# Kernel tuning notes

Measured on AMD Instinct MI355X. Metric: run time of the kernel, lower is better.

The kernel has to match this reference:

```python
import jax, jax.numpy as jnp
import numpy as np

POOL = (4000, 4000, 4000)
N_GO = 12000
N_GENES = 20000
IN_F = 8
F = 64
B = 8
D_ATT = 5
L_DIM = 16
N_LAST = 4000
EPS = 1e-5


def _seg(v, ids, n):
    # v: [B, E, ...] -> segment-sum over axis 1
    return jax.vmap(lambda a: jax.ops.segment_sum(a, ids, num_segments=n))(v)


def _ln_nodes(x, g, b):
    # torch does LayerNorm(N) on x.permute(0,2,1): normalize over the NODE axis
    mu = x.mean(axis=1, keepdims=True)
    var = x.var(axis=1, keepdims=True)
    return (x - mu) * jax.lax.rsqrt(var + EPS) * g[None, :, None] + b[None, :, None]


def _bn(x, g, b):
    # BatchNorm1d, training-mode statistics (biased var); channel axis = 1
    if x.ndim == 2:
        mu = x.mean(axis=0)
        var = x.var(axis=0)
        return (x - mu) * jax.lax.rsqrt(var + EPS) * g + b
    mu = x.mean(axis=(0, 2), keepdims=True)
    var = x.var(axis=(0, 2), keepdims=True)
    return (x - mu) * jax.lax.rsqrt(var + EPS) * g[None, :, None] + b[None, :, None]


def _enc(x, src, dst, n, w_inc, w_s, w_att_in, w_att_s, g, b):
    x_in = x @ w_inc.T                 # [B,n,F]
    x_s = x @ w_s.T
    f1 = w_inc.shape[0]
    # W_att_in([x_src; x_dst]) == x_src @ W[:, :f1].T + x_dst @ W[:, f1:].T (GAT trick)
    a_src = x_in @ w_att_in[0, :f1]    # [B,n]
    a_dst = x_in @ w_att_in[0, f1:]
    v = jnp.exp(jnp.tanh(a_src[:, src] + a_dst[:, dst]))   # [B,E]
    vn = v / _seg(v, src, n)[:, src]                        # row-normalized attention
    x_incoming = _seg(vn[:, :, None] * x_in[:, dst, :], src, n)
    v_s = jax.nn.sigmoid(x_s @ w_att_s[0])                  # [B,n]
    out = x_incoming + x_s * v_s[:, :, None]
    return jax.nn.relu(_ln_nodes(out, g, b))


def _dec(x, src, dst, n_rows, offset, w_out, w_sout, g, b):
    x_out = x @ w_out.T
    x_s = x @ w_sout.T
    deg = jax.ops.segment_sum(jnp.ones(src.shape, x.dtype), src, num_segments=n_rows)
    v = 1.0 / deg[src]                                      # [E]
    x_outgoing = _seg(v[None, :, None] * x_out[:, dst, :], src, n_rows)
    out = x_outgoing.at[:, offset:, :].add(x_s)
    return jax.nn.relu(_ln_nodes(out, g, b))


def _forward(data, t, t_D,
             w_inc0, w_inc1, w_s0, w_s1, w_att_in0, w_att_in1, w_att_s0, w_att_s1,
             gb_g0, gb_b0, gb_g1, gb_b1,
             w_out0, w_out1, w_sout0, w_sout1,
             gbd_g0, gbd_b0, gbd_g1, gbd_b1,
             catt_w, catt_bn_g, catt_bn_b,
             conc_w, b_bn_g, b_bn_b,
             concd_w, bd_bn_g, bd_bn_b,
             lat_w1, lat_bn1_g, lat_bn1_b, lat_w2, lat_bn2_g, lat_bn2_b,
             Ag_row, Ag_col,
             enc_src0, enc_dst0, enc_src1, enc_dst1,
             dec_src0, dec_dst0, dec_src1, dec_dst1):
    # initial SNP->GO sparse embedding, one sparse matrix per input channel
    gathered = data[:, Ag_col]                         # [B,nnz]
    msg0 = gathered[:, :, None] * t.T[None, :, :]      # [B,nnz,IN_F]
    x = _seg(msg0, Ag_row, N_GO)                       # [B,N_GO,IN_F]

    # encoder (attention GCN + pooling)
    x = _enc(x, enc_src0, enc_dst0, N_GO, w_inc0, w_s0, w_att_in0, w_att_s0, gb_g0, gb_b0)
    x = x[:, POOL[0]:, :]
    x = _enc(x, enc_src1, enc_dst1, N_GO - POOL[0], w_inc1, w_s1, w_att_in1, w_att_s1, gb_g1, gb_b1)
    x = x[:, POOL[1]:, :]                              # [B,N_LAST,F]

    atten_out = jax.nn.relu(_bn(x @ catt_w.T, catt_bn_g, catt_bn_b))   # [B,N_LAST,D_ATT]
    inp_out = jax.nn.relu(_bn((x @ conc_w.T)[..., 0], b_bn_g, b_bn_b)) # [B,N_LAST]

    # decoder (degree-normalized unpooling)
    x = _dec(x, dec_src0, dec_dst0, POOL[1] + POOL[2], POOL[1], w_out0, w_sout0, gbd_g0, gbd_b0)
    x = _dec(x, dec_src1, dec_dst1, N_GO, POOL[0], w_out1, w_sout1, gbd_g1, gbd_b1)

    out_D = jax.nn.relu(_bn((x @ concd_w.T)[..., 0], bd_bn_g, bd_bn_b))  # [B,N_GO]
    x_D = _seg(out_D[:, Ag_row] * t_D[None, :], Ag_col, N_GENES)          # [B,N_GENES]

    h = jax.nn.relu(_bn(inp_out @ lat_w1.T, lat_bn1_g, lat_bn1_b))
    latent = jax.nn.relu(_bn(h @ lat_w2.T, lat_bn2_g, lat_bn2_b))         # [B,L_DIM]
    return latent, x_D, atten_out


def setup_inputs():
    rng = np.random.default_rng(0)
    # GO-GO adjacency edges (row-major unique, like coalesce)
    e = np.unique(rng.integers(0, N_GO, 144000).astype(np.int64) * N_GO
                  + rng.integers(0, N_GO, 144000))
    r = (e // N_GO).astype(np.int32)
    c = (e % N_GO).astype(np.int32)
    p0, p1 = POOL[0], POOL[0] + POOL[1]
    m = (r >= p0) & (c >= p0)
    enc_src1, enc_dst1 = r[m] - p0, c[m] - p0
    ti, tj = c, r                                  # edges of A.T
    m0 = (ti >= p0) & (tj >= p1)
    dec_src0, dec_dst0 = ti[m0] - p0, tj[m0] - p1
    m1 = tj >= p0
    dec_src1, dec_dst1 = ti[m1], tj[m1] - p0
    # gene <-> GO incidence
    eg = np.unique(rng.integers(0, N_GO, 240000).astype(np.int64) * N_GENES
                   + rng.integers(0, N_GENES, 240000))
    Ag_row = (eg // N_GENES).astype(np.int32)
    Ag_col = (eg % N_GENES).astype(np.int32)
    nnz = Ag_row.shape[0]

    ks = iter(jax.random.split(jax.random.key(0), 40))

    def nrm(shape, s=0.05):
        return jax.random.normal(next(ks), shape, jnp.float32) * s

    return {
        'data': nrm((B, N_GENES), 1.0),
        't': 1.0 + nrm((IN_F, nnz), 0.1),
        't_D': 1.0 + nrm((nnz,), 0.1),
        'w_inc0': nrm((F, IN_F)), 'w_inc1': nrm((F, F)),
        'w_s0': nrm((F, IN_F)), 'w_s1': nrm((F, F)),
        'w_att_in0': nrm((1, 2 * F)), 'w_att_in1': nrm((1, 2 * F)),
        'w_att_s0': nrm((1, F)), 'w_att_s1': nrm((1, F)),
        'gb_g0': jnp.ones(N_GO), 'gb_b0': jnp.zeros(N_GO),
        'gb_g1': jnp.ones(N_GO - p0), 'gb_b1': jnp.zeros(N_GO - p0),
        'w_out0': nrm((F, F)), 'w_out1': nrm((IN_F, F)),
        'w_sout0': nrm((F, F)), 'w_sout1': nrm((IN_F, F)),
        'gbd_g0': jnp.ones(POOL[1] + POOL[2]), 'gbd_b0': jnp.zeros(POOL[1] + POOL[2]),
        'gbd_g1': jnp.ones(N_GO), 'gbd_b1': jnp.zeros(N_GO),
        'catt_w': nrm((D_ATT, F)), 'catt_bn_g': jnp.ones(N_LAST), 'catt_bn_b': jnp.zeros(N_LAST),
        'conc_w': nrm((1, F)), 'b_bn_g': jnp.ones(N_LAST), 'b_bn_b': jnp.zeros(N_LAST),
        'concd_w': nrm((1, IN_F)), 'bd_bn_g': jnp.ones(N_GO), 'bd_bn_b': jnp.zeros(N_GO),
        'lat_w1': nrm((32, N_LAST)), 'lat_bn1_g': jnp.ones(32), 'lat_bn1_b': jnp.zeros(32),
        'lat_w2': nrm((L_DIM, 32)), 'lat_bn2_g': jnp.ones(L_DIM), 'lat_bn2_b': jnp.zeros(L_DIM),
        'Ag_row': jnp.asarray(Ag_row), 'Ag_col': jnp.asarray(Ag_col),
        'enc_src0': jnp.asarray(r), 'enc_dst0': jnp.asarray(c),
        'enc_src1': jnp.asarray(enc_src1), 'enc_dst1': jnp.asarray(enc_dst1),
        'dec_src0': jnp.asarray(dec_src0), 'dec_dst0': jnp.asarray(dec_dst0),
        'dec_src1': jnp.asarray(dec_src1), 'dec_dst1': jnp.asarray(dec_dst1),
    }


def reference(data, t, t_D,
              w_inc0, w_inc1, w_s0, w_s1, w_att_in0, w_att_in1, w_att_s0, w_att_s1,
              gb_g0, gb_b0, gb_g1, gb_b1,
              w_out0, w_out1, w_sout0, w_sout1,
              gbd_g0, gbd_b0, gbd_g1, gbd_b1,
              catt_w, catt_bn_g, catt_bn_b,
              conc_w, b_bn_g, b_bn_b,
              concd_w, bd_bn_g, bd_bn_b,
              lat_w1, lat_bn1_g, lat_bn1_b, lat_w2, lat_bn2_g, lat_bn2_b,
              Ag_row, Ag_col,
              enc_src0, enc_dst0, enc_src1, enc_dst1,
              dec_src0, dec_dst0, dec_src1, dec_dst1):
    return _forward(data, t, t_D,
                    w_inc0, w_inc1, w_s0, w_s1, w_att_in0, w_att_in1, w_att_s0, w_att_s1,
                    gb_g0, gb_b0, gb_g1, gb_b1,
                    w_out0, w_out1, w_sout0, w_sout1,
                    gbd_g0, gbd_b0, gbd_g1, gbd_b1,
                    catt_w, catt_bn_g, catt_bn_b,
                    conc_w, b_bn_g, b_bn_b,
                    concd_w, bd_bn_g, bd_bn_b,
                    lat_w1, lat_bn1_g, lat_bn1_b, lat_w2, lat_bn2_g, lat_bn2_b,
                    Ag_row, Ag_col,
                    enc_src0, enc_dst0, enc_src1, enc_dst1,
                    dec_src0, dec_dst0, dec_src1, dec_dst1)
```

## Files before the change

kernel.cpp:

```cpp
#include <hip/hip_runtime.h>
#include <math.h>

#define BB 8
#define N_GO 12000
#define N_GENES 20000
#define IN_F 8
#define FF 64
#define D_ATT 5
#define L_DIM 16
#define N_LAST 4000
#define P0_ 4000
#define EPSF 1e-5f

__global__ void k_row_bounds(const int* __restrict__ src, int* __restrict__ rs,
                             int* __restrict__ re, int E) {
    int e = blockIdx.x * 256 + threadIdx.x;
    if (e >= E) return;
    int r = src[e];
    if (e == 0 || src[e - 1] != r) rs[r] = e;
    if (e == E - 1 || src[e + 1] != r) re[r] = e + 1;
}

__global__ void k_gene2go_w(const float* __restrict__ data, const float* __restrict__ t,
                            const int* __restrict__ col, const int* __restrict__ rs,
                            const int* __restrict__ re, float* __restrict__ x0, int nnz) {
    int wid = blockIdx.x * 4 + (threadIdx.x >> 6);
    if (wid >= N_GO) return;
    int lane = threadIdx.x & 63;
    int f = lane & 7, eo = lane >> 3;
    int e0 = rs[wid], e1 = re[wid];
    float acc[BB];
#pragma unroll
    for (int b = 0; b < BB; b++) acc[b] = 0.f;
    for (int e = e0; e < e1; e += 8) {
        int ee = e + eo;
        bool ok = ee < e1;
        int ec = ok ? ee : (e1 - 1);
        int c = col[ec];
        float tv = ok ? t[(size_t)f * nnz + ee] : 0.f;
#pragma unroll
        for (int b = 0; b < BB; b++)
            acc[b] += tv * data[b * N_GENES + c];
    }
#pragma unroll
    for (int b = 0; b < BB; b++) {
        acc[b] += __shfl_xor(acc[b], 8);
        acc[b] += __shfl_xor(acc[b], 16);
        acc[b] += __shfl_xor(acc[b], 32);
    }
    if (lane < IN_F) {
#pragma unroll
        for (int b = 0; b < BB; b++)
            x0[((size_t)b * N_GO + wid) * IN_F + lane] = acc[b];
    }
}

template<int FIN, bool SCAL>
__global__ __launch_bounds__(256, 2)
void k_linear2_att(const float* __restrict__ X, const float* __restrict__ W1,
                   const float* __restrict__ W2, const float* __restrict__ watt,
                   const float* __restrict__ ws, float* __restrict__ Y1,
                   float* __restrict__ Y2, float* __restrict__ ASRC,
                   float* __restrict__ ADST, float* __restrict__ VS,
                   int n_nodes, long xbs, int xoff, int total_waves) {
    __shared__ float w1s[FIN * FF];
    __shared__ float w2s[FIN * FF];
    int lane = threadIdx.x & 63;
    for (int i = threadIdx.x; i < FIN * FF; i += 256) {
        int fo = i / FIN, k = i % FIN;
        w1s[k * FF + fo] = W1[i];
        w2s[k * FF + fo] = W2[i];
    }
    __syncthreads();
    float w1r[FIN], w2r[FIN];
#pragma unroll
    for (int k = 0; k < FIN; k++) {
        w1r[k] = w1s[k * FF + lane];
        w2r[k] = w2s[k * FF + lane];
    }
    float wa = 0.f, wb = 0.f, wc = 0.f;
    if (SCAL) { wa = watt[lane]; wb = watt[FF + lane]; wc = ws[lane]; }
    int wid = blockIdx.x * 4 + (threadIdx.x >> 6);
    for (int n = wid; n < n_nodes; n += total_waves) {
        for (int b = 0; b < BB; b++) {
            const float* xr = X + (size_t)b * xbs + (size_t)(n + xoff) * FIN;
            float a1 = 0.f, a2 = 0.f;
#pragma unroll
            for (int k = 0; k < FIN; k += 4) {
                float4 x = *(const float4*)(xr + k);
                a1 += x.x * w1r[k] + x.y * w1r[k + 1] + x.z * w1r[k + 2] + x.w * w1r[k + 3];
                a2 += x.x * w2r[k] + x.y * w2r[k + 1] + x.z * w2r[k + 2] + x.w * w2r[k + 3];
            }
            Y1[((size_t)b * n_nodes + n) * FF + lane] = a1;
            Y2[((size_t)b * n_nodes + n) * FF + lane] = a2;
            if (SCAL) {
                float s0 = a1 * wa, s1 = a1 * wb, s2 = a2 * wc;
                for (int m = 1; m < 64; m <<= 1) {
                    s0 += __shfl_xor(s0, m);
                    s1 += __shfl_xor(s1, m);
                    s2 += __shfl_xor(s2, m);
                }
                if (lane == 0) {
                    ASRC[b * n_nodes + n] = s0;
                    ADST[b * n_nodes + n] = s1;
                    VS[b * n_nodes + n] = 1.f / (1.f + expf(-s2));
                }
            }
        }
    }
}

__global__ __launch_bounds__(256, 2)
void k_linear2_reg8(const float* __restrict__ X, const float* __restrict__ W1,
                    const float* __restrict__ W2, float* __restrict__ Y1,
                    float* __restrict__ Y2, int n_nodes, long xbs, int xoff,
                    int total_waves) {
    __shared__ float w1s[FF * IN_F];
    __shared__ float w2s[FF * IN_F];
    int lane = threadIdx.x & 63;
    for (int i = threadIdx.x; i < FF * IN_F; i += 256) {
        int fo = i / FF, k = i % FF;
        w1s[k * IN_F + fo] = W1[i];
        w2s[k * IN_F + fo] = W2[i];
    }
    __syncthreads();
    int of = lane & 7;
    int slot = lane >> 3;
    float w1r[FF], w2r[FF];
#pragma unroll
    for (int k = 0; k < FF; k++) {
        w1r[k] = w1s[k * IN_F + of];
        w2r[k] = w2s[k * IN_F + of];
    }
    int wid = blockIdx.x * 4 + (threadIdx.x >> 6);
    for (long n0 = (long)wid * 8; n0 < n_nodes; n0 += (long)total_waves * 8) {
        int n = (int)n0 + slot;
        bool ok = (n < n_nodes);
        int nn = ok ? n : (n_nodes - 1);
        for (int b = 0; b < BB; b++) {
            const float* xr = X + (size_t)b * xbs + (size_t)(nn + xoff) * FF;
            float a1 = 0.f, a2 = 0.f;
#pragma unroll
            for (int k = 0; k < FF; k += 4) {
                float4 x = *(const float4*)(xr + k);
                a1 += x.x * w1r[k] + x.y * w1r[k + 1] + x.z * w1r[k + 2] + x.w * w1r[k + 3];
                a2 += x.x * w2r[k] + x.y * w2r[k + 1] + x.z * w2r[k + 2] + x.w * w2r[k + 3];
            }
            if (ok) {
                Y1[((size_t)b * n_nodes + n) * IN_F + of] = a1;
                Y2[((size_t)b * n_nodes + n) * IN_F + of] = a2;
            }
        }
    }
}

__global__ void k_edge_v(const float* __restrict__ a_src, const float* __restrict__ a_dst,
                         const int* __restrict__ src, const int* __restrict__ dst,
                         float* __restrict__ v, int E, int n_nodes) {
    int e = blockIdx.x * 256 + threadIdx.x;
    if (e >= E) return;
    int b = blockIdx.y;
    v[(size_t)b * E + e] = expf(tanhf(a_src[b * n_nodes + src[e]] + a_dst[b * n_nodes + dst[e]]));
}

__global__ void k_agg_enc_f(const float* __restrict__ Xin, const float* __restrict__ Xs,
                            const float* __restrict__ EDGEV, const float* __restrict__ VS,
                            const int* __restrict__ dst, const int* __restrict__ rs,
                            const int* __restrict__ re, float* __restrict__ Out,
                            float* __restrict__ sums, int n_nodes, int E, int nblk) {
    int b = blockIdx.x & 7;
    int wid = threadIdx.x >> 6;
    int lane = threadIdx.x & 63;
    const float* Xb  = Xin + (size_t)b * n_nodes * FF;
    const float* Xsb = Xs  + (size_t)b * n_nodes * FF;
    const float* vv  = EDGEV + (size_t)b * E;
    float s1 = 0.f, s2 = 0.f;
    for (int r = (blockIdx.x >> 3) * 4 + wid; r < n_nodes; r += nblk * 4) {
        int e0 = rs[r], e1 = re[r];
        float sv0 = 0.f, sv1 = 0.f, acc0 = 0.f, acc1 = 0.f;
        int e = e0;
        for (; e + 1 < e1; e += 2) {
            int d0 = dst[e], d1 = dst[e + 1];
            float v0 = vv[e], v1 = vv[e + 1];
            sv0 += v0; sv1 += v1;
            acc0 += v0 * Xb[(size_t)d0 * FF + lane];
            acc1 += v1 * Xb[(size_t)d1 * FF + lane];
        }
        if (e < e1) {
            int d0 = dst[e];
            float v0 = vv[e];
            sv0 += v0;
            acc0 += v0 * Xb[(size_t)d0 * FF + lane];
        }
        float sv = sv0 + sv1, acc = acc0 + acc1;
        float o = (e1 > e0) ? acc / sv : 0.f;
        o += Xsb[(size_t)r * FF + lane] * VS[b * n_nodes + r];
        Out[((size_t)b * n_nodes + r) * FF + lane] = o;
        s1 += o; s2 += o * o;
    }
    __shared__ float sh1[4][64], sh2[4][64];
    sh1[wid][lane] = s1; sh2[wid][lane] = s2;
    __syncthreads();
    if (wid == 0) {
        float a = sh1[0][lane] + sh1[1][lane] + sh1[2][lane] + sh1[3][lane];
        float c = sh2[0][lane] + sh2[1][lane] + sh2[2][lane] + sh2[3][lane];
        atomicAdd(&sums[(b * FF + lane) * 2],     a);
        atomicAdd(&sums[(b * FF + lane) * 2 + 1], c);
    }
}

__global__ void k_ln_stats(const float* __restrict__ X, float* __restrict__ sums,
                           int n_nodes, int Fdim, int npb) {
    int b = blockIdx.y;
    int f = threadIdx.x & (Fdim - 1);
    int nl = threadIdx.x / Fdim;
    int stride = 256 / Fdim;
    int n0 = blockIdx.x * npb;
    int n1 = n0 + npb; if (n1 > n_nodes) n1 = n_nodes;
    const float* xb = X + (size_t)b * n_nodes * Fdim;
    float s1 = 0.f, s2 = 0.f;
    for (int n = n0 + nl; n < n1; n += stride) {
        float x = xb[(size_t)n * Fdim + f];
        s1 += x; s2 += x * x;
    }
    __shared__ float sh1[256], sh2[256];
    sh1[threadIdx.x] = s1; sh2[threadIdx.x] = s2;
    __syncthreads();
    for (int o = 128; o >= Fdim; o >>= 1) {
        if (threadIdx.x < o) { sh1[threadIdx.x] += sh1[threadIdx.x + o]; sh2[threadIdx.x] += sh2[threadIdx.x + o]; }
        __syncthreads();
    }
    if (threadIdx.x < Fdim) {
        atomicAdd(&sums[(b * Fdim + threadIdx.x) * 2],     sh1[threadIdx.x]);
        atomicAdd(&sums[(b * Fdim + threadIdx.x) * 2 + 1], sh2[threadIdx.x]);
    }
}

__global__ void k_ln_apply_relu(const float* __restrict__ X, const float* __restrict__ sums,
                                const float* __restrict__ g, const float* __restrict__ bb,
                                float* __restrict__ Y, int n_nodes, int Fdim) {
    long idx = (long)blockIdx.x * 256 + threadIdx.x;
    if (idx >= (long)n_nodes * Fdim) return;
    int b = blockIdx.y;
    int n = (int)(idx / Fdim);
    int f = (int)(idx % Fdim);
    float s1 = sums[(b * Fdim + f) * 2], s2 = sums[(b * Fdim + f) * 2 + 1];
    float mu = s1 / n_nodes;
    float var = s2 / n_nodes - mu * mu;
    float rs = rsqrtf(var + EPSF);
    size_t o = (size_t)b * n_nodes * Fdim + idx;
    float y = (X[o] - mu) * rs * g[n] + bb[n];
    Y[o] = fmaxf(y, 0.f);
}

__global__ void k_deg_i(const int* __restrict__ src, int* __restrict__ deg, int E) {
    int e = blockIdx.x * 256 + threadIdx.x;
    if (e < E) atomicAdd(&deg[src[e]], 1);
}

__global__ void k_scan(const int* __restrict__ deg, int* __restrict__ rsd,
                       int* __restrict__ cursor, int n) {
    __shared__ int part[1024];
    int t = threadIdx.x;
    int chunk = (n + 1023) >> 10;
    int s0 = t * chunk, s1 = s0 + chunk; if (s1 > n) s1 = n;
    int s = 0;
    for (int i = s0; i < s1 && i < n; i++) s += deg[i];
    part[t] = s;
    __syncthreads();
    for (int o = 1; o < 1024; o <<= 1) {
        int v = (t >= o) ? part[t - o] : 0;
        __syncthreads();
        part[t] += v;
        __syncthreads();
    }
    int base = (t == 0) ? 0 : part[t - 1];
    for (int i = s0; i < s1 && i < n; i++) {
        rsd[i] = base; cursor[i] = base;
        base += deg[i];
    }
    if (t == 1023) rsd[n] = part[1023];
}

__global__ void k_scatter(const int* __restrict__ src, const int* __restrict__ dst,
                          int* __restrict__ cursor, int* __restrict__ csrd, int E) {
    int e = blockIdx.x * 256 + threadIdx.x;
    if (e >= E) return;
    int pos = atomicAdd(&cursor[src[e]], 1);
    csrd[pos] = dst[e];
}

__global__ void k_scatter2(const int* __restrict__ key, const int* __restrict__ row,
                           const float* __restrict__ tD, int* __restrict__ cursor,
                           int* __restrict__ csrr, float* __restrict__ csrt, int E) {
    int e = blockIdx.x * 256 + threadIdx.x;
    if (e >= E) return;
    int pos = atomicAdd(&cursor[key[e]], 1);
    csrr[pos] = row[e];
    csrt[pos] = tD[e];
}

__global__ void k_xd_g(const float* __restrict__ outD, const int* __restrict__ rsg,
                       const int* __restrict__ csrr, const float* __restrict__ csrt,
                       float* __restrict__ xD) {
    int g = blockIdx.x * 4 + (threadIdx.x >> 6);
    if (g >= N_GENES) return;
    int lane = threadIdx.x & 63;
    int b = lane & 7, slot = lane >> 3;
    int e0 = rsg[g], e1 = rsg[g + 1];
    float acc = 0.f;
    for (int e = e0 + slot; e < e1; e += 8)
        acc += csrt[e] * outD[(size_t)b * N_GO + csrr[e]];
    acc += __shfl_xor(acc, 8);
    acc += __shfl_xor(acc, 16);
    acc += __shfl_xor(acc, 32);
    if (lane < BB)
        xD[(size_t)b * N_GENES + g] = acc;
}

__global__ void k_agg_dec64(const float* __restrict__ Xout, const float* __restrict__ Xs,
                            const int* __restrict__ rsd, const int* __restrict__ csrd,
                            float* __restrict__ Out, float* __restrict__ sums,
                            int n_rows, int n_in, int offset, int nblk) {
    int b = blockIdx.x & 7;
    int wid = threadIdx.x >> 6;
    int lane = threadIdx.x & 63;
    const float* Xb = Xout + (size_t)b * n_in * FF;
    int nxs = n_rows - offset;
    const float* Xsb = Xs + (size_t)b * nxs * FF;
    float s1 = 0.f, s2 = 0.f;
    for (int r = (blockIdx.x >> 3) * 4 + wid; r < n_rows; r += nblk * 4) {
        int e0 = rsd[r], e1 = rsd[r + 1];
        float acc0 = 0.f, acc1 = 0.f;
        int e = e0;
        for (; e + 1 < e1; e += 2) {
            acc0 += Xb[(size_t)csrd[e] * FF + lane];
            acc1 += Xb[(size_t)csrd[e + 1] * FF + lane];
        }
        if (e < e1) acc0 += Xb[(size_t)csrd[e] * FF + lane];
        float acc = acc0 + acc1;
        float o = (e1 > e0) ? acc / (float)(e1 - e0) : 0.f;
        if (r >= offset)
            o += Xsb[(size_t)(r - offset) * FF + lane];
        Out[((size_t)b * n_rows + r) * FF + lane] = o;
        s1 += o; s2 += o * o;
    }
    __shared__ float sh1[4][64], sh2[4][64];
    sh1[wid][lane] = s1; sh2[wid][lane] = s2;
    __syncthreads();
    if (wid == 0) {
        float a = sh1[0][lane] + sh1[1][lane] + sh1[2][lane] + sh1[3][lane];
        float c = sh2[0][lane] + sh2[1][lane] + sh2[2][lane] + sh2[3][lane];
        atomicAdd(&sums[(b * FF + lane) * 2],     a);
        atomicAdd(&sums[(b * FF + lane) * 2 + 1], c);
    }
}

__global__ void k_agg_dec8(const float* __restrict__ Xout, const float* __restrict__ Xs,
                           const int* __restrict__ rsd, const int* __restrict__ csrd,
                           float* __restrict__ Out, int n_rows, int n_in, int offset) {
    int r = blockIdx.x * 4 + (threadIdx.x >> 6);
    if (r >= n_rows) return;
    int lane = threadIdx.x & 63;
    int f = lane & 7, slot = lane >> 3;
    int e0 = rsd[r], e1 = rsd[r + 1];
    float acc[BB];
#pragma unroll
    for (int b = 0; b < BB; b++) acc[b] = 0.f;
    for (int e = e0 + slot; e < e1; e += 8) {
        int d = csrd[e];
#pragma unroll
        for (int b = 0; b < BB; b++)
            acc[b] += Xout[((size_t)b * n_in + d) * IN_F + f];
    }
#pragma unroll
    for (int b = 0; b < BB; b++) {
        acc[b] += __shfl_xor(acc[b], 8);
        acc[b] += __shfl_xor(acc[b], 16);
        acc[b] += __shfl_xor(acc[b], 32);
    }
    float coef = (e1 > e0) ? 1.f / (float)(e1 - e0) : 0.f;
    int nxs = n_rows - offset;
    if (lane < IN_F) {
#pragma unroll
        for (int b = 0; b < BB; b++) {
            float o = acc[b] * coef;
            if (r >= offset)
                o += Xs[((size_t)b * nxs + (r - offset)) * IN_F + lane];
            Out[((size_t)b * n_rows + r) * IN_F + lane] = o;
        }
    }
}

__global__ void k_heads(const float* __restrict__ X, const float* __restrict__ Wa,
                        const float* __restrict__ wc, const float* __restrict__ ga,
                        const float* __restrict__ ba, const float* __restrict__ gc,
                        const float* __restrict__ bc, float* __restrict__ ATT,
                        float* __restrict__ INP, long xbs, int xoff) {
    int i = blockIdx.x * 4 + (threadIdx.x >> 6);
    if (i >= N_LAST) return;
    int lane = threadIdx.x & 63;
    float w0 = Wa[0 * FF + lane], w1 = Wa[1 * FF + lane], w2 = Wa[2 * FF + lane];
    float w3 = Wa[3 * FF + lane], w4 = Wa[4 * FF + lane];
    float wcv = wc[lane];
    float y[BB][D_ATT], yc[BB];
    float s1 = 0.f, s2 = 0.f;
#pragma unroll
    for (int b = 0; b < BB; b++) {
        float x = X[(size_t)b * xbs + (size_t)(i + xoff) * FF + lane];
        float p0 = x * w0, p1 = x * w1, p2 = x * w2, p3 = x * w3, p4 = x * w4, pc = x * wcv;
        for (int m = 1; m < 64; m <<= 1) {
            p0 += __shfl_xor(p0, m); p1 += __shfl_xor(p1, m); p2 += __shfl_xor(p2, m);
            p3 += __shfl_xor(p3, m); p4 += __shfl_xor(p4, m); pc += __shfl_xor(pc, m);
        }
        y[b][0] = p0; y[b][1] = p1; y[b][2] = p2; y[b][3] = p3; y[b][4] = p4;
        yc[b] = pc;
        s1 += p0 + p1 + p2 + p3 + p4;
        s2 += p0 * p0 + p1 * p1 + p2 * p2 + p3 * p3 + p4 * p4;
    }
    const float cnt = (float)(BB * D_ATT);
    float mu = s1 / cnt, var = s2 / cnt - mu * mu;
    float rsv = rsqrtf(var + EPSF);
    float gg = ga[i], bv = ba[i];
#pragma unroll
    for (int b = 0; b < BB; b++) {
        float yv = lane == 0 ? y[b][0] : lane == 1 ? y[b][1] : lane == 2 ? y[b][2]
                 : lane == 3 ? y[b][3] : y[b][4];
        if (lane < D_ATT)
            ATT[((size_t)b * N_LAST + i) * D_ATT + lane] = fmaxf((yv - mu) * rsv * gg + bv, 0.f);
    }
    float c1 = 0.f, c2 = 0.f;
#pragma unroll
    for (int b = 0; b < BB; b++) { c1 += yc[b]; c2 += yc[b] * yc[b]; }
    float muc = c1 / BB, varc = c2 / BB - muc * muc;
    float rc = rsqrtf(varc + EPSF);
    float ggc = gc[i], bvc = bc[i];
    if (lane < BB) {
        float v = lane == 0 ? yc[0] : lane == 1 ? yc[1] : lane == 2 ? yc[2] : lane == 3 ? yc[3]
                : lane == 4 ? yc[4] : lane == 5 ? yc[5] : lane == 6 ? yc[6] : yc[7];
        INP[(size_t)lane * N_LAST + i] = fmaxf((v - muc) * rc * ggc + bvc, 0.f);
    }
}

template<int FIN>
__global__ void k_head_scalar(const float* __restrict__ X, const float* __restrict__ w,
                              const float* __restrict__ g, const float* __restrict__ bb,
                              float* __restrict__ Z, int n_nodes, long xbs, int xoff) {
    int i = blockIdx.x * 256 + threadIdx.x;
    if (i >= n_nodes) return;
    float y[BB];
    float s1 = 0.f, s2 = 0.f;
    const float4* wr = (const float4*)w;
    for (int b = 0; b < BB; b++) {
        const float4* xr = (const float4*)(X + (size_t)b * xbs + (size_t)(i + xoff) * FIN);
        float acc = 0.f;
#pragma unroll
        for (int q = 0; q < FIN / 4; q++) {
            float4 x = xr[q], u = wr[q];
            acc += x.x * u.x + x.y * u.y + x.z * u.z + x.w * u.w;
        }
        y[b] = acc; s1 += acc; s2 += acc * acc;
    }
    float mu = s1 / BB, var = s2 / BB - mu * mu;
    float rs = rsqrtf(var + EPSF);
    float gg = g[i], bv = bb[i];
    for (int b = 0; b < BB; b++)
        Z[(size_t)b * n_nodes + i] = fmaxf((y[b] - mu) * rs * gg + bv, 0.f);
}

__global__ void k_lat1(const float* __restrict__ INP, const float* __restrict__ W,
                       const float* __restrict__ g, const float* __restrict__ bb,
                       float* __restrict__ H1R) {
    int j = blockIdx.x;
    int w = threadIdx.x >> 6;
    int lane = threadIdx.x & 63;
    const float* xr = INP + (size_t)w * N_LAST;
    const float* wr = W + (size_t)j * N_LAST;
    float s = 0.f;
    for (int k = lane; k < N_LAST; k += 64) s += xr[k] * wr[k];
    for (int o = 32; o > 0; o >>= 1) s += __shfl_down(s, o);
    __shared__ float sh[BB];
    if (lane == 0) sh[w] = s;
    __syncthreads();
    if (threadIdx.x < BB) {
        float s1 = 0.f, s2 = 0.f;
        for (int q = 0; q < BB; q++) { float y = sh[q]; s1 += y; s2 += y * y; }
        float mu = s1 / BB, var = s2 / BB - mu * mu;
        float rs = rsqrtf(var + EPSF);
        H1R[threadIdx.x * 32 + j] = fmaxf((sh[threadIdx.x] - mu) * rs * g[j] + bb[j], 0.f);
    }
}

__global__ void k_lat2(const float* __restrict__ H1R, const float* __restrict__ W2,
                       const float* __restrict__ g, const float* __restrict__ bb,
                       float* __restrict__ out_lat) {
    int b = threadIdx.x >> 4, j = threadIdx.x & 15;
    float acc = 0.f;
    for (int k = 0; k < 32; k++) acc += H1R[b * 32 + k] * W2[j * 32 + k];
    __shared__ float sh[128];
    sh[threadIdx.x] = acc;
    __syncthreads();
    float s1 = 0.f, s2 = 0.f;
    for (int q = 0; q < BB; q++) { float y = sh[q * 16 + j]; s1 += y; s2 += y * y; }
    float mu = s1 / BB, var = s2 / BB - mu * mu;
    float rs = rsqrtf(var + EPSF);
    out_lat[b * 16 + j] = fmaxf((acc - mu) * rs * g[j] + bb[j], 0.f);
}

extern "C" void kernel_launch(void* const* d_in, const int* in_sizes, int n_in,
                              void* d_out, int out_size, void* d_ws, size_t ws_size,
                              hipStream_t stream) {
    const float* data      = (const float*)d_in[0];
    const float* t         = (const float*)d_in[1];
    const float* t_D       = (const float*)d_in[2];
    const float* w_inc0    = (const float*)d_in[3];
    const float* w_inc1    = (const float*)d_in[4];
    const float* w_s0      = (const float*)d_in[5];
    const float* w_s1      = (const float*)d_in[6];
    const float* w_att_in0 = (const float*)d_in[7];
    const float* w_att_in1 = (const float*)d_in[8];
    const float* w_att_s0  = (const float*)d_in[9];
    const float* w_att_s1  = (const float*)d_in[10];
    const float* gb_g0     = (const float*)d_in[11];
    const float* gb_b0     = (const float*)d_in[12];
    const float* gb_g1     = (const float*)d_in[13];
    const float* gb_b1     = (const float*)d_in[14];
    const float* w_out0    = (const float*)d_in[15];
    const float* w_out1    = (const float*)d_in[16];
    const float* w_sout0   = (const float*)d_in[17];
    const float* w_sout1   = (const float*)d_in[18];
    const float* gbd_g0    = (const float*)d_in[19];
    const float* gbd_b0    = (const float*)d_in[20];
    const float* gbd_g1    = (const float*)d_in[21];
    const float* gbd_b1    = (const float*)d_in[22];
    const float* catt_w    = (const float*)d_in[23];
    const float* catt_bn_g = (const float*)d_in[24];
    const float* catt_bn_b = (const float*)d_in[25];
    const float* conc_w    = (const float*)d_in[26];
    const float* b_bn_g    = (const float*)d_in[27];
    const float* b_bn_b    = (const float*)d_in[28];
    const float* concd_w   = (const float*)d_in[29];
    const float* bd_bn_g   = (const float*)d_in[30];
    const float* bd_bn_b   = (const float*)d_in[31];
    const float* lat_w1    = (const float*)d_in[32];
    const float* lat_bn1_g = (const float*)d_in[33];
    const float* lat_bn1_b = (const float*)d_in[34];
    const float* lat_w2    = (const float*)d_in[35];
    const float* lat_bn2_g = (const float*)d_in[36];
    const float* lat_bn2_b = (const float*)d_in[37];
    const int* Ag_row   = (const int*)d_in[38];
    const int* Ag_col   = (const int*)d_in[39];
    const int* enc_src0 = (const int*)d_in[40];
    const int* enc_dst0 = (const int*)d_in[41];
    const int* enc_src1 = (const int*)d_in[42];
    const int* enc_dst1 = (const int*)d_in[43];
    const int* dec_src0 = (const int*)d_in[44];
    const int* dec_dst0 = (const int*)d_in[45];
    const int* dec_src1 = (const int*)d_in[46];
    const int* dec_dst1 = (const int*)d_in[47];

    const int nnz = in_sizes[2];
    const int E0  = in_sizes[40];
    const int E1  = in_sizes[42];
    const int ED0 = in_sizes[44];
    const int ED1 = in_sizes[46];
    int EDMAX = (ED0 > ED1 ? ED0 : ED1);
    if (nnz > EDMAX) EDMAX = nnz;

    char* wsb = (char*)d_ws;
    size_t off = 0;
    auto alloc = [&](size_t bytes) -> void* {
        void* p = wsb + off;
        off += (bytes + 255) & ~(size_t)255;
        return p;
    };
    const size_t ARENA = (size_t)BB * N_GO * FF;
    float* P0 = (float*)alloc(ARENA * 4);
    float* P1 = (float*)alloc(ARENA * 4);
    float* P2 = (float*)alloc(ARENA * 4);
    float* P3 = (float*)alloc(ARENA * 4);
    float* EDGEV = (float*)alloc((size_t)BB * E0 * 4);
    float* ASRC = (float*)alloc((size_t)BB * N_GO * 4);
    float* ADST = (float*)alloc((size_t)BB * N_GO * 4);
    float* VS   = (float*)alloc((size_t)BB * N_GO * 4);
    float* SUMS = (float*)alloc(2 * BB * FF * 4);
    float* INP  = (float*)alloc((size_t)BB * N_LAST * 4);
    float* OUTD = (float*)alloc((size_t)BB * N_GO * 4);
    float* H1R  = (float*)alloc(BB * 32 * 4);
    int* RS   = (int*)alloc(N_GO * 4);
    int* RE   = (int*)alloc(N_GO * 4);
    int* DEGI = (int*)alloc(N_GENES * 4);
    int* RSD  = (int*)alloc((N_GENES + 1) * 4);
    int* CURS = (int*)alloc(N_GENES * 4);
    int* CSRD = (int*)alloc((size_t)EDMAX * 4);
    float* CSRT = (float*)alloc((size_t)nnz * 4);

    float* out_lat = (float*)d_out;
    float* out_xd  = out_lat + BB * L_DIM;
    float* out_att = out_xd + (size_t)BB * N_GENES;

    dim3 blk(256);
    auto g1 = [](long n) { return dim3((unsigned)((n + 255) / 256)); };
    auto g2 = [](long n, int y) { return dim3((unsigned)((n + 255) / 256), (unsigned)y); };
    auto gw = [](int n) { return dim3((unsigned)((n + 3) / 4)); };
    const int LNB = 1024;
    const int LWAVES = LNB * 4;
    const int ANB = 256;
    const int N1 = N_GO - P0_;

    hipMemsetAsync(RS, 0, N_GO * 4, stream);
    hipMemsetAsync(RE, 0, N_GO * 4, stream);
    k_row_bounds<<<g1(nnz), blk, 0, stream>>>(Ag_row, RS, RE, nnz);
    k_gene2go_w<<<gw(N_GO), blk, 0, stream>>>(data, t, Ag_col, RS, RE, P0, nnz);

    k_linear2_att<IN_F, true><<<dim3(LNB), blk, 0, stream>>>(P0, w_inc0, w_s0, w_att_in0, w_att_s0,
        P1, P2, ASRC, ADST, VS, N_GO, (long)N_GO * IN_F, 0, LWAVES);
    hipMemsetAsync(RS, 0, N_GO * 4, stream);
    hipMemsetAsync(RE, 0, N_GO * 4, stream);
    k_row_bounds<<<g1(E0), blk, 0, stream>>>(enc_src0, RS, RE, E0);
    k_edge_v<<<g2(E0, BB), blk, 0, stream>>>(ASRC, ADST, enc_src0, enc_dst0, EDGEV, E0, N_GO);
    hipMemsetAsync(SUMS, 0, 2 * BB * FF * 4, stream);
    k_agg_enc_f<<<dim3(ANB * 8), blk, 0, stream>>>(P1, P2, EDGEV, VS, enc_dst0, RS, RE, P3, SUMS, N_GO, E0, ANB);
    k_ln_apply_relu<<<g2((long)N_GO * FF, BB), blk, 0, stream>>>(P3, SUMS, gb_g0, gb_b0, P0, N_GO, FF);

    k_linear2_att<FF, true><<<dim3(LNB), blk, 0, stream>>>(P0, w_inc1, w_s1, w_att_in1, w_att_s1,
        P1, P2, ASRC, ADST, VS, N1, (long)N_GO * FF, P0_, LWAVES);
    hipMemsetAsync(RS, 0, N_GO * 4, stream);
    hipMemsetAsync(RE, 0, N_GO * 4, stream);
    k_row_bounds<<<g1(E1), blk, 0, stream>>>(enc_src1, RS, RE, E1);
    k_edge_v<<<g2(E1, BB), blk, 0, stream>>>(ASRC, ADST, enc_src1, enc_dst1, EDGEV, E1, N1);
    hipMemsetAsync(SUMS, 0, 2 * BB * FF * 4, stream);
    k_agg_enc_f<<<dim3(ANB * 8), blk, 0, stream>>>(P1, P2, EDGEV, VS, enc_dst1, RS, RE, P3, SUMS, N1, E1, ANB);
    k_ln_apply_relu<<<g2((long)N1 * FF, BB), blk, 0, stream>>>(P3, SUMS, gb_g1, gb_b1, P0, N1, FF);

    k_heads<<<gw(N_LAST), blk, 0, stream>>>(P0, catt_w, conc_w, catt_bn_g, catt_bn_b,
                                            b_bn_g, b_bn_b, out_att, INP, (long)N1 * FF, P0_);

    k_linear2_att<FF, false><<<dim3(LNB), blk, 0, stream>>>(P0, w_out0, w_sout0, nullptr, nullptr,
        P1, P2, nullptr, nullptr, nullptr, N_LAST, (long)N1 * FF, P0_, LWAVES);
    hipMemsetAsync(DEGI, 0, 8000 * 4, stream);
    k_deg_i<<<g1(ED0), blk, 0, stream>>>(dec_src0, DEGI, ED0);
    k_scan<<<dim3(1), dim3(1024), 0, stream>>>(DEGI, RSD, CURS, 8000);
    k_scatter<<<g1(ED0), blk, 0, stream>>>(dec_src0, dec_dst0, CURS, CSRD, ED0);
    hipMemsetAsync(SUMS, 0, 2 * BB * FF * 4, stream);
    k_agg_dec64<<<dim3(ANB * 8), blk, 0, stream>>>(P1, P2, RSD, CSRD, P3, SUMS, 8000, N_LAST, 4000, ANB);
    k_ln_apply_relu<<<g2((long)8000 * FF, BB), blk, 0, stream>>>(P3, SUMS, gbd_g0, gbd_b0, P0, 8000, FF);

    k_linear2_reg8<<<dim3(LNB), blk, 0, stream>>>(P0, w_out1, w_sout1, P1, P2, 8000, (long)8000 * FF, 0, LWAVES);
    hipMemsetAsync(DEGI, 0, N_GO * 4, stream);
    k_deg_i<<<g1(ED1), blk, 0, stream>>>(dec_src1, DEGI, ED1);
    k_scan<<<dim3(1), dim3(1024), 0, stream>>>(DEGI, RSD, CURS, N_GO);
    k_scatter<<<g1(ED1), blk, 0, stream>>>(dec_src1, dec_dst1, CURS, CSRD, ED1);
    k_agg_dec8<<<gw(N_GO), blk, 0, stream>>>(P1, P2, RSD, CSRD, P3, N_GO, 8000, 4000);
    hipMemsetAsync(SUMS, 0, 2 * BB * IN_F * 4, stream);
    k_ln_stats<<<dim3((N_GO + 511) / 512, BB), blk, 0, stream>>>(P3, SUMS, N_GO, IN_F, 512);
    k_ln_apply_relu<<<g2((long)N_GO * IN_F, BB), blk, 0, stream>>>(P3, SUMS, gbd_g1, gbd_b1, P0, N_GO, IN_F);

    k_head_scalar<IN_F><<<g1(N_GO), blk, 0, stream>>>(P0, concd_w, bd_bn_g, bd_bn_b, OUTD, N_GO, (long)N_GO * IN_F, 0);
    hipMemsetAsync(DEGI, 0, N_GENES * 4, stream);
    k_deg_i<<<g1(nnz), blk, 0, stream>>>(Ag_col, DEGI, nnz);
    k_scan<<<dim3(1), dim3(1024), 0, stream>>>(DEGI, RSD, CURS, N_GENES);
    k_scatter2<<<g1(nnz), blk, 0, stream>>>(Ag_col, Ag_row, t_D, CURS, CSRD, CSRT, nnz);
    k_xd_g<<<gw(N_GENES), blk, 0, stream>>>(OUTD, RSD, CSRD, CSRT, out_xd);

    k_lat1<<<dim3(32), dim3(512), 0, stream>>>(INP, lat_w1, lat_bn1_g, lat_bn1_b, H1R);
    k_lat2<<<dim3(1), dim3(128), 0, stream>>>(H1R, lat_w2, lat_bn2_g, lat_bn2_b, out_lat);

    (void)n_in; (void)out_size; (void)ws_size;
}
```

Measured before the change: 544.2 us.

## Binary-search row bounds, transpose gene data, unroll gather loops by four

Replaces the memset-plus-scan row-bounds kernels with a per-row binary search over the sorted source array, which removes two memsets per stage. Adds a small transpose of the gene data so each column gather reads eight batch values as two float4 loads instead of eight strided loads. Unrolls the encoder and decoder edge aggregation loops to four independent accumulators so more gathers are in flight at once. The trade-off is one extra transpose kernel and buffer, plus somewhat higher register use in the aggregation kernels.

```diff
diff --git a/kernel.cpp b/kernel.cpp
--- a/kernel.cpp
+++ b/kernel.cpp
@@ -12,16 +12,26 @@
 #define P0_ 4000
 #define EPSF 1e-5f
 
-__global__ void k_row_bounds(const int* __restrict__ src, int* __restrict__ rs,
-                             int* __restrict__ re, int E) {
-    int e = blockIdx.x * 256 + threadIdx.x;
-    if (e >= E) return;
-    int r = src[e];
-    if (e == 0 || src[e - 1] != r) rs[r] = e;
-    if (e == E - 1 || src[e + 1] != r) re[r] = e + 1;
-}
-
-__global__ void k_gene2go_w(const float* __restrict__ data, const float* __restrict__ t,
+__global__ void k_bounds_bs(const int* __restrict__ src, int* __restrict__ rs,
+                            int* __restrict__ re, int E, int n) {
+    int r = blockIdx.x * 256 + threadIdx.x;
+    if (r >= n) return;
+    int lo = 0, hi = E;
+    while (lo < hi) { int m = (lo + hi) >> 1; if (src[m] < r) lo = m + 1; else hi = m; }
+    rs[r] = lo;
+    int lo2 = lo, hi2 = E;
+    while (lo2 < hi2) { int m = (lo2 + hi2) >> 1; if (src[m] < r + 1) lo2 = m + 1; else hi2 = m; }
+    re[r] = lo2;
+}
+
+__global__ void k_tr_data(const float* __restrict__ data, float* __restrict__ dataT) {
+    int idx = blockIdx.x * 256 + threadIdx.x;
+    if (idx >= N_GENES * BB) return;
+    int g = idx >> 3, b = idx & 7;
+    dataT[idx] = data[b * N_GENES + g];
+}
+
+__global__ void k_gene2go_w(const float* __restrict__ dataT, const float* __restrict__ t,
                             const int* __restrict__ col, const int* __restrict__ rs,
                             const int* __restrict__ re, float* __restrict__ x0, int nnz) {
     int wid = blockIdx.x * 4 + (threadIdx.x >> 6);
@@ -38,9 +48,10 @@
         int ec = ok ? ee : (e1 - 1);
         int c = col[ec];
         float tv = ok ? t[(size_t)f * nnz + ee] : 0.f;
-#pragma unroll
-        for (int b = 0; b < BB; b++)
-            acc[b] += tv * data[b * N_GENES + c];
+        const float4* dt = (const float4*)(dataT + (size_t)c * 8);
+        float4 d0 = dt[0], d1 = dt[1];
+        acc[0] += tv * d0.x; acc[1] += tv * d0.y; acc[2] += tv * d0.z; acc[3] += tv * d0.w;
+        acc[4] += tv * d1.x; acc[5] += tv * d1.y; acc[6] += tv * d1.z; acc[7] += tv * d1.w;
     }
 #pragma unroll
     for (int b = 0; b < BB; b++) {
@@ -177,22 +188,26 @@
     float s1 = 0.f, s2 = 0.f;
     for (int r = (blockIdx.x >> 3) * 4 + wid; r < n_nodes; r += nblk * 4) {
         int e0 = rs[r], e1 = re[r];
-        float sv0 = 0.f, sv1 = 0.f, acc0 = 0.f, acc1 = 0.f;
+        float sv0 = 0.f, sv1 = 0.f, sv2 = 0.f, sv3 = 0.f;
+        float acc0 = 0.f, acc1 = 0.f, acc2 = 0.f, acc3 = 0.f;
         int e = e0;
-        for (; e + 1 < e1; e += 2) {
-            int d0 = dst[e], d1 = dst[e + 1];
-            float v0 = vv[e], v1 = vv[e + 1];
-            sv0 += v0; sv1 += v1;
+        for (; e + 3 < e1; e += 4) {
+            int d0 = dst[e], d1 = dst[e + 1], d2 = dst[e + 2], d3 = dst[e + 3];
+            float v0 = vv[e], v1 = vv[e + 1], v2 = vv[e + 2], v3 = vv[e + 3];
+            sv0 += v0; sv1 += v1; sv2 += v2; sv3 += v3;
             acc0 += v0 * Xb[(size_t)d0 * FF + lane];
             acc1 += v1 * Xb[(size_t)d1 * FF + lane];
-        }
-        if (e < e1) {
+            acc2 += v2 * Xb[(size_t)d2 * FF + lane];
+            acc3 += v3 * Xb[(size_t)d3 * FF + lane];
+        }
+        for (; e < e1; e++) {
             int d0 = dst[e];
             float v0 = vv[e];
             sv0 += v0;
             acc0 += v0 * Xb[(size_t)d0 * FF + lane];
         }
-        float sv = sv0 + sv1, acc = acc0 + acc1;
+        float sv = (sv0 + sv1) + (sv2 + sv3);
+        float acc = (acc0 + acc1) + (acc2 + acc3);
         float o = (e1 > e0) ? acc / sv : 0.f;
         o += Xsb[(size_t)r * FF + lane] * VS[b * n_nodes + r];
         Out[((size_t)b * n_nodes + r) * FF + lane] = o;
@@ -331,14 +346,16 @@
     float s1 = 0.f, s2 = 0.f;
     for (int r = (blockIdx.x >> 3) * 4 + wid; r < n_rows; r += nblk * 4) {
         int e0 = rsd[r], e1 = rsd[r + 1];
-        float acc0 = 0.f, acc1 = 0.f;
+        float acc0 = 0.f, acc1 = 0.f, acc2 = 0.f, acc3 = 0.f;
         int e = e0;
-        for (; e + 1 < e1; e += 2) {
+        for (; e + 3 < e1; e += 4) {
             acc0 += Xb[(size_t)csrd[e] * FF + lane];
             acc1 += Xb[(size_t)csrd[e + 1] * FF + lane];
-        }
-        if (e < e1) acc0 += Xb[(size_t)csrd[e] * FF + lane];
-        float acc = acc0 + acc1;
+            acc2 += Xb[(size_t)csrd[e + 2] * FF + lane];
+            acc3 += Xb[(size_t)csrd[e + 3] * FF + lane];
+        }
+        for (; e < e1; e++) acc0 += Xb[(size_t)csrd[e] * FF + lane];
+        float acc = (acc0 + acc1) + (acc2 + acc3);
         float o = (e1 > e0) ? acc / (float)(e1 - e0) : 0.f;
         if (r >= offset)
             o += Xsb[(size_t)(r - offset) * FF + lane];
@@ -587,6 +604,7 @@
     float* INP  = (float*)alloc((size_t)BB * N_LAST * 4);
     float* OUTD = (float*)alloc((size_t)BB * N_GO * 4);
     float* H1R  = (float*)alloc(BB * 32 * 4);
+    float* DATAT = (float*)alloc((size_t)N_GENES * BB * 4);
     int* RS   = (int*)alloc(N_GO * 4);
     int* RE   = (int*)alloc(N_GO * 4);
     int* DEGI = (int*)alloc(N_GENES * 4);
@@ -608,16 +626,13 @@
     const int ANB = 256;
     const int N1 = N_GO - P0_;
 
-    hipMemsetAsync(RS, 0, N_GO * 4, stream);
-    hipMemsetAsync(RE, 0, N_GO * 4, stream);
-    k_row_bounds<<<g1(nnz), blk, 0, stream>>>(Ag_row, RS, RE, nnz);
-    k_gene2go_w<<<gw(N_GO), blk, 0, stream>>>(data, t, Ag_col, RS, RE, P0, nnz);
+    k_tr_data<<<g1(N_GENES * BB), blk, 0, stream>>>(data, DATAT);
+    k_bounds_bs<<<g1(N_GO), blk, 0, stream>>>(Ag_row, RS, RE, nnz, N_GO);
+    k_gene2go_w<<<gw(N_GO), blk, 0, stream>>>(DATAT, t, Ag_col, RS, RE, P0, nnz);
 
     k_linear2_att<IN_F, true><<<dim3(LNB), blk, 0, stream>>>(P0, w_inc0, w_s0, w_att_in0, w_att_s0,
         P1, P2, ASRC, ADST, VS, N_GO, (long)N_GO * IN_F, 0, LWAVES);
-    hipMemsetAsync(RS, 0, N_GO * 4, stream);
-    hipMemsetAsync(RE, 0, N_GO * 4, stream);
-    k_row_bounds<<<g1(E0), blk, 0, stream>>>(enc_src0, RS, RE, E0);
+    k_bounds_bs<<<g1(N_GO), blk, 0, stream>>>(enc_src0, RS, RE, E0, N_GO);
     k_edge_v<<<g2(E0, BB), blk, 0, stream>>>(ASRC, ADST, enc_src0, enc_dst0, EDGEV, E0, N_GO);
     hipMemsetAsync(SUMS, 0, 2 * BB * FF * 4, stream);
     k_agg_enc_f<<<dim3(ANB * 8), blk, 0, stream>>>(P1, P2, EDGEV, VS, enc_dst0, RS, RE, P3, SUMS, N_GO, E0, ANB);
@@ -625,9 +640,7 @@
 
     k_linear2_att<FF, true><<<dim3(LNB), blk, 0, stream>>>(P0, w_inc1, w_s1, w_att_in1, w_att_s1,
         P1, P2, ASRC, ADST, VS, N1, (long)N_GO * FF, P0_, LWAVES);
-    hipMemsetAsync(RS, 0, N_GO * 4, stream);
-    hipMemsetAsync(RE, 0, N_GO * 4, stream);
-    k_row_bounds<<<g1(E1), blk, 0, stream>>>(enc_src1, RS, RE, E1);
+    k_bounds_bs<<<g1(N1), blk, 0, stream>>>(enc_src1, RS, RE, E1, N1);
     k_edge_v<<<g2(E1, BB), blk, 0, stream>>>(ASRC, ADST, enc_src1, enc_dst1, EDGEV, E1, N1);
     hipMemsetAsync(SUMS, 0, 2 * BB * FF * 4, stream);
     k_agg_enc_f<<<dim3(ANB * 8), blk, 0, stream>>>(P1, P2, EDGEV, VS, enc_dst1, RS, RE, P3, SUMS, N1, E1, ANB);
```

Result: faster. 533.3 us (-2.0%).
